# Kernel tuning notes

Measured on AMD Instinct MI355X. Metric: run time of the kernel, lower is better.

## Reference

```python
import jax, jax.numpy as jnp
import numpy as np

RADIUS = 0.2
NSAMPLE = 32


def ball_query(new_xyz, xyz, radius, nsample):
    # new_xyz: (B, M, 3), xyz: (B, N, 3) -> idx: (B, M, nsample) int32
    B, M, _ = new_xyz.shape
    N = xyz.shape[1]
    # pairwise squared distances (B, M, N)
    diff = new_xyz[:, :, None, :] - xyz[:, None, :, :]
    dist2 = jnp.sum(diff * diff, axis=-1)
    mask = dist2 < (radius * radius)
    ar = jnp.arange(N, dtype=jnp.int32)
    masked = jnp.where(mask, ar[None, None, :], jnp.int32(N + 1))  # (B,M,N)
    sorted_idx = jnp.sort(masked, axis=2)[:, :, :nsample]          # (B,M,nsample)
    invalid = sorted_idx >= N
    first = sorted_idx[:, :, 0:1]
    idx = jnp.where(invalid, jnp.broadcast_to(first, sorted_idx.shape), sorted_idx)
    return idx


def group_points(points, idx):
    # points: (B, C, N), idx: (B, M, nsample) -> (B, C, M, nsample)
    B, C, N = points.shape
    M, ns = idx.shape[1], idx.shape[2]
    flat = jnp.broadcast_to(idx.reshape(B, 1, M * ns), (B, C, M * ns))
    return jnp.take_along_axis(points, flat, axis=2).reshape(B, C, M, ns)


def setup_inputs() -> dict:
    key = jax.random.key(0)
    k1, k2, k3 = jax.random.split(key, 3)
    xyz = jax.random.uniform(k1, (8, 16384, 3), dtype=jnp.float32)
    new_xyz = jax.random.uniform(k2, (8, 1024, 3), dtype=jnp.float32)
    features = jax.random.normal(k3, (8, 64, 16384), dtype=jnp.float32)
    return {"xyz": xyz, "new_xyz": new_xyz, "features": features}


def reference(xyz, new_xyz, features):
    idx = ball_query(new_xyz, xyz, RADIUS, NSAMPLE)          # (B,M,ns)
    xyz_t = jnp.transpose(xyz, (0, 2, 1))                    # (B,3,N)
    grouped_xyz = group_points(xyz_t, idx)                   # (B,3,M,ns)
    grouped_xyz = grouped_xyz - jnp.transpose(new_xyz, (0, 2, 1))[:, :, :, None]
    grouped_features = group_points(features, idx)           # (B,C,M,ns)
    new_features = jnp.concatenate([grouped_xyz, grouped_features], axis=1)
    return new_features                                      # (B, 3+C, M, ns)
```

## Files before the change

kernel.cpp:

```cpp
#include <hip/hip_runtime.h>


#define N_PTS   16384
#define M_Q     1024
#define B_SZ    8
#define NSAMP   32
#define NCH     64
#define R2      0.04f
#define OUT_CH  (3 + NCH)

typedef float f4 __attribute__((ext_vector_type(4)));

__global__ __launch_bounds__(256) void pack_kernel(
    const float* __restrict__ xyz, f4* __restrict__ pk)
{
    const int i = blockIdx.x * 256 + threadIdx.x;
    const float* src = xyz + (size_t)i * 3;
    f4 v;
    v.x = src[0]; v.y = src[1]; v.z = src[2]; v.w = 0.0f;
    pk[i] = v;
}

__global__ __launch_bounds__(256) void fat_kernel(
    const float* __restrict__ feat,
    const float* __restrict__ new_xyz,
    const f4*    __restrict__ pk,
    float* __restrict__ ft,
    int*   __restrict__ meta,
    float* __restrict__ out)
{
    __shared__ float tile[64][65];
    __shared__ float pxyz[4][NSAMP][4];
    const int tid  = threadIdx.x;
    const int u    = (blockIdx.x & 7) | ((blockIdx.x >> 4) << 3);
    const int type = (blockIdx.x >> 3) & 1;
    const int b    = u & 7;

    if (type == 0) {
        const int n0 = (u >> 3) << 6;
        const float* __restrict__ fb = feat + (size_t)b * NCH * N_PTS;
        float* __restrict__ tb       = ft   + ((size_t)b * N_PTS + n0) * NCH;
#pragma unroll
        for (int j = 0; j < 16; ++j) {
            const int idx = j * 256 + tid;
            const int c = idx >> 6, nn = idx & 63;
            tile[c][nn] = __builtin_nontemporal_load(&fb[(size_t)c * N_PTS + n0 + nn]);
        }
        __syncthreads();
        const int c4 = tid & 15;
        const int r  = tid >> 4;
#pragma unroll
        for (int j = 0; j < 4; ++j) {
            const int nn = j * 16 + r;
            f4 o;
            o.x = tile[c4 * 4 + 0][nn];
            o.y = tile[c4 * 4 + 1][nn];
            o.z = tile[c4 * 4 + 2][nn];
            o.w = tile[c4 * 4 + 3][nn];
            *(f4*)(&tb[(size_t)nn * NCH + c4 * 4]) = o;
        }
        return;
    }

    const int w    = tid >> 6;
    const int lane = tid & 63;
    const int m    = ((u >> 3) << 2) + w;
    const int q    = (b << 10) + m;

    const float cx = new_xyz[q * 3 + 0];
    const float cy = new_xyz[q * 3 + 1];
    const float cz = new_xyz[q * 3 + 2];
    const f4* __restrict__ pb = pk + (size_t)b * N_PTS;

    const unsigned long long lt = (1ull << lane) - 1ull;
    int cnt = 0;
    f4 PA = pb[lane];
    f4 PB = pb[64 + lane];

    for (int base = 0; ; base += 128) {
        const int  nbase = base + 128;
        const bool more  = nbase < N_PTS;
        const int  pAi = more ? nbase + lane : lane;
        const f4 nPA = pb[pAi];
        const f4 nPB = pb[pAi + 64];

        {
            const float dx = __fsub_rn(cx, PA.x), dy = __fsub_rn(cy, PA.y), dz = __fsub_rn(cz, PA.z);
            const float d2 = __fadd_rn(__fadd_rn(__fmul_rn(dx, dx), __fmul_rn(dy, dy)),
                                       __fmul_rn(dz, dz));
            const bool hit = d2 < R2;
            const unsigned long long mk = __ballot(hit);
            if (hit) {
                const int slot = cnt + __popcll(mk & lt);
                if (slot < NSAMP) {
                    pxyz[w][slot][0] = -dx;
                    pxyz[w][slot][1] = -dy;
                    pxyz[w][slot][2] = -dz;
                    pxyz[w][slot][3] = __int_as_float(base + lane);
                }
            }
            cnt += (int)__popcll(mk);
        }
        {
            const float dx = __fsub_rn(cx, PB.x), dy = __fsub_rn(cy, PB.y), dz = __fsub_rn(cz, PB.z);
            const float d2 = __fadd_rn(__fadd_rn(__fmul_rn(dx, dx), __fmul_rn(dy, dy)),
                                       __fmul_rn(dz, dz));
            const bool hit = d2 < R2;
            const unsigned long long mk = __ballot(hit);
            if (hit) {
                const int slot = cnt + __popcll(mk & lt);
                if (slot < NSAMP) {
                    pxyz[w][slot][0] = -dx;
                    pxyz[w][slot][1] = -dy;
                    pxyz[w][slot][2] = -dz;
                    pxyz[w][slot][3] = __int_as_float(base + 64 + lane);
                }
            }
            cnt += (int)__popcll(mk);
        }
        if (cnt >= NSAMP || !more) break;
        PA = nPA; PB = nPB;
    }

    if (lane < NSAMP && cnt < NSAMP) {
        float v0x, v0y, v0z, v0w;
        if (cnt > 0) {
            v0x = pxyz[w][0][0]; v0y = pxyz[w][0][1];
            v0z = pxyz[w][0][2]; v0w = pxyz[w][0][3];
        } else {
            const f4 p0 = pb[0];
            v0x = __fsub_rn(p0.x, cx); v0y = __fsub_rn(p0.y, cy);
            v0z = __fsub_rn(p0.z, cz); v0w = __int_as_float(0);
        }
        if (lane >= cnt) {
            pxyz[w][lane][0] = v0x; pxyz[w][lane][1] = v0y;
            pxyz[w][lane][2] = v0z; pxyz[w][lane][3] = v0w;
        }
    }

    float* __restrict__ ob = out + ((size_t)b * OUT_CH * M_Q + (size_t)m) * NSAMP;
    if (lane < 24) {
        const int c  = lane >> 3;
        const int s4 = lane & 7;
        f4 o;
        o.x = pxyz[w][s4 * 4 + 0][c];
        o.y = pxyz[w][s4 * 4 + 1][c];
        o.z = pxyz[w][s4 * 4 + 2][c];
        o.w = pxyz[w][s4 * 4 + 3][c];
        __builtin_nontemporal_store(o, (f4*)&ob[(size_t)c * (M_Q * NSAMP) + s4 * 4]);
    }

    if (lane < NSAMP)
        meta[(size_t)q * NSAMP + lane] = __float_as_int(pxyz[w][lane][3]);
}

__global__ __launch_bounds__(256) void group_kernel(
    const int*   __restrict__ meta,
    const float* __restrict__ ft,
    float* __restrict__ out)
{
    const int tid  = threadIdx.x;
    const int w    = tid >> 6;
    const int lane = tid & 63;
    const int b    = blockIdx.x & 7;
    const int m    = ((blockIdx.x >> 3) << 2) + w;
    const int q    = (b << 10) + m;

    __shared__ int   ishare[4][NSAMP];
    __shared__ float tile[4][32][33];

    if (lane < NSAMP)
        ishare[w][lane] = meta[(size_t)q * NSAMP + lane];

    float* __restrict__ ob = out + ((size_t)b * OUT_CH * M_Q + (size_t)m) * NSAMP;
    const float* __restrict__ ftb = ft + (size_t)b * N_PTS * NCH;
    const int sgrp = lane >> 3;
    const int c4   = lane & 7;

#pragma unroll
    for (int chunk = 0; chunk < 2; ++chunk) {
        f4 vals[4];
#pragma unroll
        for (int i = 0; i < 4; ++i) {
            const int s = i * 8 + sgrp;
            const int n = ishare[w][s];
            vals[i] = *(const f4*)(ftb + (size_t)n * NCH + chunk * 32 + c4 * 4);
        }
#pragma unroll
        for (int i = 0; i < 4; ++i) {
            const int s = i * 8 + sgrp;
            tile[w][c4 * 4 + 0][s] = vals[i].x;
            tile[w][c4 * 4 + 1][s] = vals[i].y;
            tile[w][c4 * 4 + 2][s] = vals[i].z;
            tile[w][c4 * 4 + 3][s] = vals[i].w;
        }
#pragma unroll
        for (int j = 0; j < 4; ++j) {
            const int c_loc = j * 8 + (lane >> 3);
            const int s4    = lane & 7;
            f4 o;
            o.x = tile[w][c_loc][s4 * 4 + 0];
            o.y = tile[w][c_loc][s4 * 4 + 1];
            o.z = tile[w][c_loc][s4 * 4 + 2];
            o.w = tile[w][c_loc][s4 * 4 + 3];
            __builtin_nontemporal_store(
                o, (f4*)&ob[(size_t)(3 + chunk * 32 + c_loc) * (M_Q * NSAMP) + s4 * 4]);
        }
    }
}

__global__ __launch_bounds__(256) void qg_fallback(
    const float* __restrict__ xyz, const float* __restrict__ new_xyz,
    const float* __restrict__ feat, float* __restrict__ out)
{
    const int tid  = threadIdx.x;
    const int w    = tid >> 6;
    const int lane = tid & 63;
    const int q    = blockIdx.x * 4 + w;
    const int b    = q >> 10;
    const int m    = q & (M_Q - 1);

    __shared__ int idx_sh[4][NSAMP];

    const float cx = new_xyz[q * 3 + 0];
    const float cy = new_xyz[q * 3 + 1];
    const float cz = new_xyz[q * 3 + 2];
    const float* __restrict__ xb = xyz + (size_t)b * N_PTS * 3;

    int cnt = 0;
    for (int base = 0; base < N_PTS && cnt < NSAMP; base += 64) {
        const int n = base + lane;
        const float dx = __fsub_rn(cx, xb[n * 3 + 0]);
        const float dy = __fsub_rn(cy, xb[n * 3 + 1]);
        const float dz = __fsub_rn(cz, xb[n * 3 + 2]);
        const float d2 = __fadd_rn(__fadd_rn(__fmul_rn(dx, dx), __fmul_rn(dy, dy)),
                                   __fmul_rn(dz, dz));
        const bool hit = d2 < R2;
        const unsigned long long mk = __ballot(hit);
        if (hit) {
            const int slot = cnt + __popcll(mk & ((1ull << lane) - 1ull));
            if (slot < NSAMP) idx_sh[w][slot] = n;
        }
        cnt += (int)__popcll(mk);
    }
    __syncthreads();
    if (lane < NSAMP) {
        const int v0 = (cnt > 0) ? idx_sh[w][0] : 0;
        if (lane >= cnt) idx_sh[w][lane] = v0;
    }
    __syncthreads();

    const float* __restrict__ fb = feat + (size_t)b * NCH * N_PTS;
    float* __restrict__ ob = out + ((size_t)b * OUT_CH * M_Q + (size_t)m) * NSAMP;
    for (int e = lane; e < OUT_CH * NSAMP; e += 64) {
        const int c = e >> 5, s = e & 31;
        const int n = idx_sh[w][s];
        float v;
        if (c < 3) {
            const float ctr = (c == 0) ? cx : ((c == 1) ? cy : cz);
            v = __fsub_rn(xb[n * 3 + c], ctr);
        } else {
            v = fb[(size_t)(c - 3) * N_PTS + n];
        }
        ob[(size_t)c * (M_Q * NSAMP) + s] = v;
    }
}

extern "C" void kernel_launch(void* const* d_in, const int* in_sizes, int n_in,
                              void* d_out, int out_size, void* d_ws, size_t ws_size,
                              hipStream_t stream) {
    const float* xyz     = (const float*)d_in[0];
    const float* new_xyz = (const float*)d_in[1];
    const float* feat    = (const float*)d_in[2];
    float* out           = (float*)d_out;

    const size_t ft_elems   = (size_t)B_SZ * N_PTS * NCH;
    const size_t pk_elems   = (size_t)B_SZ * N_PTS;
    const size_t meta_elems = (size_t)B_SZ * M_Q * NSAMP;
    const size_t need = ft_elems * sizeof(float) + pk_elems * sizeof(f4)
                      + meta_elems * sizeof(int);

    float* ft   = (float*)d_ws;
    f4*    pk   = (f4*)(ft + ft_elems);
    int*   meta = (int*)(pk + pk_elems);

    if (ws_size >= need) {
        pack_kernel<<<(B_SZ * N_PTS) / 256, 256, 0, stream>>>(xyz, pk);
        fat_kernel<<<4096, 256, 0, stream>>>(feat, new_xyz, pk, ft, meta, out);
        group_kernel<<<(B_SZ * M_Q) / 4, 256, 0, stream>>>(meta, ft, out);
    } else {
        qg_fallback<<<(B_SZ * M_Q) / 4, 256, 0, stream>>>(xyz, new_xyz, feat, out);
    }
}
```

Before: 127.9 us.

## Split ball-query scan across two waves per query and switch points to SoA

Each query is now scanned by two wavefronts, each covering half of the point cloud. After a block barrier the two partial hit lists are merged in order, and the merged result is written to the output and to the index metadata. Points are stored as separate x/y/z arrays instead of padded float4, which cuts point read traffic by a quarter. The grid grows from 4096 to 6144 blocks, giving more parallelism on queries that stop early. The cost is that the second half is always scanned even when the first half already has enough hits, which adds wasted work.

```diff
diff --git a/kernel.cpp b/kernel.cpp
--- a/kernel.cpp
+++ b/kernel.cpp
@@ -8,36 +8,43 @@
 #define NCH     64
 #define R2      0.04f
 #define OUT_CH  (3 + NCH)
+#define HALF_N  (N_PTS / 2)
 
 typedef float f4 __attribute__((ext_vector_type(4)));
 
-__global__ __launch_bounds__(256) void pack_kernel(
-    const float* __restrict__ xyz, f4* __restrict__ pk)
+__global__ __launch_bounds__(256) void soa_kernel(
+    const float* __restrict__ xyz,
+    float* __restrict__ xs, float* __restrict__ ys, float* __restrict__ zs)
 {
     const int i = blockIdx.x * 256 + threadIdx.x;
     const float* src = xyz + (size_t)i * 3;
-    f4 v;
-    v.x = src[0]; v.y = src[1]; v.z = src[2]; v.w = 0.0f;
-    pk[i] = v;
+    xs[i] = src[0];
+    ys[i] = src[1];
+    zs[i] = src[2];
 }
 
 __global__ __launch_bounds__(256) void fat_kernel(
     const float* __restrict__ feat,
     const float* __restrict__ new_xyz,
-    const f4*    __restrict__ pk,
+    const float* __restrict__ xs, const float* __restrict__ ys,
+    const float* __restrict__ zs,
     float* __restrict__ ft,
     int*   __restrict__ meta,
     float* __restrict__ out)
 {
     __shared__ float tile[64][65];
-    __shared__ float pxyz[4][NSAMP][4];
-    const int tid  = threadIdx.x;
-    const int u    = (blockIdx.x & 7) | ((blockIdx.x >> 4) << 3);
-    const int type = (blockIdx.x >> 3) & 1;
-    const int b    = u & 7;
-
-    if (type == 0) {
-        const int n0 = (u >> 3) << 6;
+    __shared__ float lists[2][2][NSAMP][4];
+    __shared__ int   kcnt[2][2];
+    __shared__ float fin[2][NSAMP][4];
+
+    const int tid = threadIdx.x;
+    const int b   = blockIdx.x & 7;
+    const int g   = blockIdx.x >> 3;
+    const int g3  = g / 3;
+    const int r3  = g - g3 * 3;
+
+    if (r3 == 0) {
+        const int n0 = g3 << 6;
         const float* __restrict__ fb = feat + (size_t)b * NCH * N_PTS;
         float* __restrict__ tb       = ft   + ((size_t)b * N_PTS + n0) * NCH;
 #pragma unroll
@@ -64,28 +71,35 @@
 
     const int w    = tid >> 6;
     const int lane = tid & 63;
-    const int m    = ((u >> 3) << 2) + w;
+    const int ql   = w >> 1;
+    const int h    = w & 1;
+    const int v    = g3 * 2 + (r3 - 1);
+    const int m    = v * 2 + ql;
     const int q    = (b << 10) + m;
 
     const float cx = new_xyz[q * 3 + 0];
     const float cy = new_xyz[q * 3 + 1];
     const float cz = new_xyz[q * 3 + 2];
-    const f4* __restrict__ pb = pk + (size_t)b * N_PTS;
-
+    const float* __restrict__ xsb = xs + (size_t)b * N_PTS;
+    const float* __restrict__ ysb = ys + (size_t)b * N_PTS;
+    const float* __restrict__ zsb = zs + (size_t)b * N_PTS;
+
+    const int start = h * HALF_N;
     const unsigned long long lt = (1ull << lane) - 1ull;
     int cnt = 0;
-    f4 PA = pb[lane];
-    f4 PB = pb[64 + lane];
-
-    for (int base = 0; ; base += 128) {
+    float Ax = xsb[start + lane],      Ay = ysb[start + lane],      Az = zsb[start + lane];
+    float Bx = xsb[start + 64 + lane], By = ysb[start + 64 + lane], Bz = zsb[start + 64 + lane];
+
+    for (int base = start; ; base += 128) {
         const int  nbase = base + 128;
-        const bool more  = nbase < N_PTS;
-        const int  pAi = more ? nbase + lane : lane;
-        const f4 nPA = pb[pAi];
-        const f4 nPB = pb[pAi + 64];
+        const bool more  = nbase < start + HALF_N;
+        const int  pA = more ? nbase + lane : start + lane;
+        const int  pB = pA + 64;
+        const float nAx = xsb[pA], nAy = ysb[pA], nAz = zsb[pA];
+        const float nBx = xsb[pB], nBy = ysb[pB], nBz = zsb[pB];
 
         {
-            const float dx = __fsub_rn(cx, PA.x), dy = __fsub_rn(cy, PA.y), dz = __fsub_rn(cz, PA.z);
+            const float dx = __fsub_rn(cx, Ax), dy = __fsub_rn(cy, Ay), dz = __fsub_rn(cz, Az);
             const float d2 = __fadd_rn(__fadd_rn(__fmul_rn(dx, dx), __fmul_rn(dy, dy)),
                                        __fmul_rn(dz, dz));
             const bool hit = d2 < R2;
@@ -93,16 +107,16 @@
             if (hit) {
                 const int slot = cnt + __popcll(mk & lt);
                 if (slot < NSAMP) {
-                    pxyz[w][slot][0] = -dx;
-                    pxyz[w][slot][1] = -dy;
-                    pxyz[w][slot][2] = -dz;
-                    pxyz[w][slot][3] = __int_as_float(base + lane);
+                    lists[ql][h][slot][0] = -dx;
+                    lists[ql][h][slot][1] = -dy;
+                    lists[ql][h][slot][2] = -dz;
+                    lists[ql][h][slot][3] = __int_as_float(base + lane);
                 }
             }
             cnt += (int)__popcll(mk);
         }
         {
-            const float dx = __fsub_rn(cx, PB.x), dy = __fsub_rn(cy, PB.y), dz = __fsub_rn(cz, PB.z);
+            const float dx = __fsub_rn(cx, Bx), dy = __fsub_rn(cy, By), dz = __fsub_rn(cz, Bz);
             const float d2 = __fadd_rn(__fadd_rn(__fmul_rn(dx, dx), __fmul_rn(dy, dy)),
                                        __fmul_rn(dz, dz));
             const bool hit = d2 < R2;
@@ -110,48 +124,59 @@
             if (hit) {
                 const int slot = cnt + __popcll(mk & lt);
                 if (slot < NSAMP) {
-                    pxyz[w][slot][0] = -dx;
-                    pxyz[w][slot][1] = -dy;
-                    pxyz[w][slot][2] = -dz;
-                    pxyz[w][slot][3] = __int_as_float(base + 64 + lane);
+                    lists[ql][h][slot][0] = -dx;
+                    lists[ql][h][slot][1] = -dy;
+                    lists[ql][h][slot][2] = -dz;
+                    lists[ql][h][slot][3] = __int_as_float(base + 64 + lane);
                 }
             }
             cnt += (int)__popcll(mk);
         }
         if (cnt >= NSAMP || !more) break;
-        PA = nPA; PB = nPB;
-    }
-
-    if (lane < NSAMP && cnt < NSAMP) {
-        float v0x, v0y, v0z, v0w;
-        if (cnt > 0) {
-            v0x = pxyz[w][0][0]; v0y = pxyz[w][0][1];
-            v0z = pxyz[w][0][2]; v0w = pxyz[w][0][3];
+        Ax = nAx; Ay = nAy; Az = nAz;
+        Bx = nBx; By = nBy; Bz = nBz;
+    }
+    if (lane == 0) kcnt[ql][h] = (cnt < NSAMP) ? cnt : NSAMP;
+
+    __syncthreads();
+
+    if (h == 0 && lane < NSAMP) {
+        const int k0 = kcnt[ql][0];
+        const int k1 = kcnt[ql][1];
+        float e0, e1, e2, e3;
+        int src_h, src_s;
+        if (lane < k0)           { src_h = 0; src_s = lane; }
+        else if (lane - k0 < k1) { src_h = 1; src_s = lane - k0; }
+        else if (k0 > 0)         { src_h = 0; src_s = 0; }
+        else if (k1 > 0)         { src_h = 1; src_s = 0; }
+        else                     { src_h = -1; src_s = 0; }
+        if (src_h >= 0) {
+            e0 = lists[ql][src_h][src_s][0];
+            e1 = lists[ql][src_h][src_s][1];
+            e2 = lists[ql][src_h][src_s][2];
+            e3 = lists[ql][src_h][src_s][3];
         } else {
-            const f4 p0 = pb[0];
-            v0x = __fsub_rn(p0.x, cx); v0y = __fsub_rn(p0.y, cy);
-            v0z = __fsub_rn(p0.z, cz); v0w = __int_as_float(0);
-        }
-        if (lane >= cnt) {
-            pxyz[w][lane][0] = v0x; pxyz[w][lane][1] = v0y;
-            pxyz[w][lane][2] = v0z; pxyz[w][lane][3] = v0w;
-        }
-    }
-
-    float* __restrict__ ob = out + ((size_t)b * OUT_CH * M_Q + (size_t)m) * NSAMP;
-    if (lane < 24) {
+            e0 = __fsub_rn(xsb[0], cx); e1 = __fsub_rn(ysb[0], cy);
+            e2 = __fsub_rn(zsb[0], cz); e3 = __int_as_float(0);
+        }
+        meta[(size_t)q * NSAMP + lane] = __float_as_int(e3);
+        fin[ql][lane][0] = e0;
+        fin[ql][lane][1] = e1;
+        fin[ql][lane][2] = e2;
+        fin[ql][lane][3] = e3;
+    }
+
+    if (h == 0 && lane < 24) {
         const int c  = lane >> 3;
         const int s4 = lane & 7;
+        float* __restrict__ ob = out + ((size_t)b * OUT_CH * M_Q + (size_t)m) * NSAMP;
         f4 o;
-        o.x = pxyz[w][s4 * 4 + 0][c];
-        o.y = pxyz[w][s4 * 4 + 1][c];
-        o.z = pxyz[w][s4 * 4 + 2][c];
-        o.w = pxyz[w][s4 * 4 + 3][c];
+        o.x = fin[ql][s4 * 4 + 0][c];
+        o.y = fin[ql][s4 * 4 + 1][c];
+        o.z = fin[ql][s4 * 4 + 2][c];
+        o.w = fin[ql][s4 * 4 + 3][c];
         __builtin_nontemporal_store(o, (f4*)&ob[(size_t)c * (M_Q * NSAMP) + s4 * 4]);
     }
-
-    if (lane < NSAMP)
-        meta[(size_t)q * NSAMP + lane] = __float_as_int(pxyz[w][lane][3]);
 }
 
 __global__ __launch_bounds__(256) void group_kernel(
@@ -275,18 +300,20 @@
     float* out           = (float*)d_out;
 
     const size_t ft_elems   = (size_t)B_SZ * N_PTS * NCH;
-    const size_t pk_elems   = (size_t)B_SZ * N_PTS;
+    const size_t soa_elems  = (size_t)B_SZ * N_PTS;
     const size_t meta_elems = (size_t)B_SZ * M_Q * NSAMP;
-    const size_t need = ft_elems * sizeof(float) + pk_elems * sizeof(f4)
+    const size_t need = (ft_elems + 3 * soa_elems) * sizeof(float)
                       + meta_elems * sizeof(int);
 
     float* ft   = (float*)d_ws;
-    f4*    pk   = (f4*)(ft + ft_elems);
-    int*   meta = (int*)(pk + pk_elems);
+    float* xs   = ft + ft_elems;
+    float* ys   = xs + soa_elems;
+    float* zs   = ys + soa_elems;
+    int*   meta = (int*)(zs + soa_elems);
 
     if (ws_size >= need) {
-        pack_kernel<<<(B_SZ * N_PTS) / 256, 256, 0, stream>>>(xyz, pk);
-        fat_kernel<<<4096, 256, 0, stream>>>(feat, new_xyz, pk, ft, meta, out);
+        soa_kernel<<<(B_SZ * N_PTS) / 256, 256, 0, stream>>>(xyz, xs, ys, zs);
+        fat_kernel<<<6144, 256, 0, stream>>>(feat, new_xyz, xs, ys, zs, ft, meta, out);
         group_kernel<<<(B_SZ * M_Q) / 4, 256, 0, stream>>>(meta, ft, out);
     } else {
         qg_fallback<<<(B_SZ * M_Q) / 4, 256, 0, stream>>>(xyz, new_xyz, feat, out);
```

Measured after the change: 131.1 us. +2.5%, slower.
